# Kernel optimization log

Measured on AMD Instinct MI355X. Metric: run time of the kernel, lower is better.

## Reference

```python
import jax, jax.numpy as jnp
import numpy as np

NUM_Q = 10000
DK = 128   # dim_key (width of each memory slot and of embeddings)
DV = 64    # dim_value (number of memory slots)
B = 128
S = 200


def setup_inputs() -> dict:
    key = jax.random.key(0)
    ks = jax.random.split(key, 16)
    sc = 0.05
    return {
        "question_seq": jax.random.randint(ks[0], (B, S), 0, NUM_Q),
        "correct_seq": jax.random.randint(ks[1], (B, S), 0, 2),
        "k_emb": jax.random.normal(ks[2], (NUM_Q, DK), jnp.float32) * sc,
        "v_emb": jax.random.normal(ks[3], (2 * NUM_Q, DK), jnp.float32) * sc,
        "Mk": jax.random.normal(ks[4], (DV, DK), jnp.float32) * sc,
        "Mv0": jax.random.normal(ks[5], (DV, DK), jnp.float32) * sc,
        "fW": jax.random.normal(ks[6], (2 * DK, DK), jnp.float32) * sc,
        "fb": jnp.zeros((DK,), jnp.float32),
        "eW": jax.random.normal(ks[7], (DK, DK), jnp.float32) * sc,
        "eb": jnp.zeros((DK,), jnp.float32),
        "aW": jax.random.normal(ks[8], (DK, DK), jnp.float32) * sc,
        "ab": jnp.zeros((DK,), jnp.float32),
        "pW": jax.random.normal(ks[9], (DK, 1), jnp.float32) * sc,
        "pb": jnp.zeros((1,), jnp.float32),
    }


def reference(question_seq, correct_seq, k_emb, v_emb, Mk, Mv0, fW, fb, eW, eb, aW, ab, pW, pb):
    num_q = k_emb.shape[0]
    x = question_seq + num_q * correct_seq            # [B,S]
    k = k_emb[question_seq]                           # [B,S,DK]
    v = v_emb[x]                                      # [B,S,DK]

    w = jax.nn.softmax(jnp.einsum('bsk,vk->bsv', k, Mk), axis=-1)  # [B,S,DV]
    e = jax.nn.sigmoid(v @ eW + eb)                   # [B,S,DK]
    a = jnp.tanh(v @ aW + ab)                         # [B,S,DK]

    Mvt0 = jnp.broadcast_to(Mv0[None], (question_seq.shape[0],) + Mv0.shape)  # [B,DV,DK]

    def step(Mvt, inp):
        wt, et, at = inp                              # [B,DV],[B,DK],[B,DK]
        read = jnp.einsum('bv,bvk->bk', wt, Mvt)      # read BEFORE update (Mv[:, :-1])
        we = wt[:, :, None] * et[:, None, :]          # [B,DV,DK]
        wa = wt[:, :, None] * at[:, None, :]
        Mvt_new = Mvt * (1.0 - we) + wa
        return Mvt_new, read

    xs = (w.transpose(1, 0, 2), e.transpose(1, 0, 2), a.transpose(1, 0, 2))
    _, reads = jax.lax.scan(step, Mvt0, xs)           # reads: [S,B,DK]
    reads = reads.transpose(1, 0, 2)                  # [B,S,DK]

    f = jnp.tanh(jnp.concatenate([reads, k], axis=-1) @ fW + fb)  # [B,S,DK]
    # dropout is identity in eval mode
    predict_score = jax.nn.sigmoid(f @ pW + pb).squeeze(-1)       # [B,S]
    return predict_score
```

## Files before the change

kernel.cpp:

```cpp
#include <hip/hip_runtime.h>
#include <math.h>


typedef float f32x4 __attribute__((ext_vector_type(4)));
typedef short bf16x8 __attribute__((ext_vector_type(8)));

__device__ __forceinline__ float sigm(float x) { return 1.0f / (1.0f + __expf(-x)); }
__device__ __forceinline__ float ftanh(float x) {
    x = fminf(20.f, fmaxf(-20.f, x));
    const float t = __expf(2.0f * x);
    return (t - 1.0f) / (t + 1.0f);
}
__device__ __forceinline__ short f2bf(float x) {
    union { float f; unsigned u; } v; v.f = x;
    return (short)((v.u + 0x7FFFu + ((v.u >> 16) & 1u)) >> 16);
}

__global__ __launch_bounds__(256) void prep_kernel(
    const float* __restrict__ eW, const float* __restrict__ aW,
    const float* __restrict__ fW, const float* __restrict__ Mk,
    short* __restrict__ eWt, short* __restrict__ aWt,
    short* __restrict__ fWrt, short* __restrict__ fWkt,
    short* __restrict__ Mkb)
{
    const int t = threadIdx.x;
    if (blockIdx.x == 4) {
        for (int idx = t; idx < 1024; idx += 256) {
            const int row = idx >> 4, c8 = idx & 15;
            const float4 f0 = *(const float4*)(Mk + row * 128 + c8 * 8);
            const float4 f1 = *(const float4*)(Mk + row * 128 + c8 * 8 + 4);
            bf16x8 v;
            v[0] = f2bf(f0.x); v[1] = f2bf(f0.y); v[2] = f2bf(f0.z); v[3] = f2bf(f0.w);
            v[4] = f2bf(f1.x); v[5] = f2bf(f1.y); v[6] = f2bf(f1.z); v[7] = f2bf(f1.w);
            *(bf16x8*)(Mkb + row * 128 + c8 * 8) = v;
        }
        return;
    }
    const float* src; short* dst;
    switch (blockIdx.x) {
        case 0:  src = eW;             dst = eWt;  break;
        case 1:  src = aW;             dst = aWt;  break;
        case 2:  src = fW;             dst = fWrt; break;
        default: src = fW + 128 * 128; dst = fWkt; break;
    }
    const int n  = t & 127;
    const int kh = (t >> 7) * 64;
    for (int k0 = kh; k0 < kh + 64; k0 += 8) {
        bf16x8 v;
        #pragma unroll
        for (int kk = 0; kk < 8; ++kk) v[kk] = f2bf(src[(k0 + kk) * 128 + n]);
        *(bf16x8*)(dst + n * 128 + k0) = v;
    }
}

__global__ __launch_bounds__(256) void veakf_kernel(
    const float* __restrict__ v_emb, const float* __restrict__ k_emb,
    const short* __restrict__ eWt, const short* __restrict__ aWt,
    const short* __restrict__ fWkt, const short* __restrict__ Mkb,
    const float* __restrict__ eb, const float* __restrict__ ab,
    const float* __restrict__ fb,
    int num_q, int nbe, int nbk,
    float* __restrict__ e_all, float* __restrict__ a_all,
    float* __restrict__ kf_all, float* __restrict__ w_all)
{
    __shared__ __align__(16) short Bsh[128 * 128];
    const int t = threadIdx.x;
    const int bid = blockIdx.x;
    int type, R0;
    if (bid < nbe)                { type = 0; R0 = bid * 64; }
    else if (bid < 2 * nbe)       { type = 1; R0 = (bid - nbe) * 64; }
    else if (bid < 2 * nbe + nbk) { type = 2; R0 = (bid - 2 * nbe) * 64; }
    else                          { type = 3; R0 = (bid - 2 * nbe - nbk) * 64; }
    const bool ea = (type < 2);
    const int nrows = ea ? 2 * num_q : num_q;
    const float* Asrc = ea ? v_emb : k_emb;

    const int wv = t >> 6;
    const int lr = t & 15;
    const int lk = (t & 63) >> 4;
    const int arow = wv * 16 + lr;
    int gr = R0 + arow; if (gr > nrows - 1) gr = nrows - 1;

    float4 a0[4], a1[4];
    #pragma unroll
    for (int ks = 0; ks < 4; ++ks) {
        const int off = (ks * 4 + lk) * 8;
        a0[ks] = *(const float4*)(Asrc + (size_t)gr * 128 + off);
        a1[ks] = *(const float4*)(Asrc + (size_t)gr * 128 + off + 4);
    }
    {
        const short* Bt = (type == 0) ? eWt : (type == 1) ? aWt
                        : (type == 2) ? fWkt : Mkb;
        const int niter = (type == 3) ? 4 : 8;
        for (int i = 0; i < niter; ++i) {
            const int c = t + 256 * i;
            const int row = c >> 4, ch = c & 15;
            *(bf16x8*)&Bsh[row * 128 + ((ch ^ (row & 7)) * 8)] =
                *(const bf16x8*)(Bt + row * 128 + ch * 8);
        }
    }
    bf16x8 af[4];
    #pragma unroll
    for (int ks = 0; ks < 4; ++ks) {
        bf16x8 v;
        v[0] = f2bf(a0[ks].x); v[1] = f2bf(a0[ks].y);
        v[2] = f2bf(a0[ks].z); v[3] = f2bf(a0[ks].w);
        v[4] = f2bf(a1[ks].x); v[5] = f2bf(a1[ks].y);
        v[6] = f2bf(a1[ks].z); v[7] = f2bf(a1[ks].w);
        af[ks] = v;
    }
    __syncthreads();

    if (type == 3) {
        f32x4 accw[4];
        #pragma unroll
        for (int ct = 0; ct < 4; ++ct) accw[ct] = (f32x4)0.f;
        #pragma unroll
        for (int ks = 0; ks < 4; ++ks) {
            const int chunk = ks * 4 + lk;
            #pragma unroll
            for (int ct = 0; ct < 4; ++ct) {
                const int n = ct * 16 + lr;
                const bf16x8 b = *(const bf16x8*)&Bsh[n * 128 + ((chunk ^ (n & 7)) * 8)];
                accw[ct] = __builtin_amdgcn_mfma_f32_16x16x32_bf16(af[ks], b, accw[ct], 0, 0, 0);
            }
        }
        #pragma unroll
        for (int r = 0; r < 4; ++r) {
            const float x0 = accw[0][r], x1 = accw[1][r];
            const float x2 = accw[2][r], x3 = accw[3][r];
            float m = fmaxf(fmaxf(x0, x1), fmaxf(x2, x3));
            #pragma unroll
            for (int mk = 1; mk < 16; mk <<= 1) m = fmaxf(m, __shfl_xor(m, mk));
            const float e0 = __expf(x0 - m), e1 = __expf(x1 - m);
            const float e2 = __expf(x2 - m), e3 = __expf(x3 - m);
            float s = (e0 + e1) + (e2 + e3);
            #pragma unroll
            for (int mk = 1; mk < 16; mk <<= 1) s += __shfl_xor(s, mk);
            const float inv = 1.0f / s;
            const int row = R0 + wv * 16 + lk * 4 + r;
            if (row < nrows) {
                float* wr = w_all + (size_t)row * 64 + lr;
                wr[0]  = e0 * inv; wr[16] = e1 * inv;
                wr[32] = e2 * inv; wr[48] = e3 * inv;
            }
        }
        return;
    }

    f32x4 acc[8];
    #pragma unroll
    for (int ct = 0; ct < 8; ++ct) acc[ct] = (f32x4)0.f;
    #pragma unroll
    for (int ks = 0; ks < 4; ++ks) {
        const int chunk = ks * 4 + lk;
        #pragma unroll
        for (int ct = 0; ct < 8; ++ct) {
            const int n = ct * 16 + lr;
            const bf16x8 b = *(const bf16x8*)&Bsh[n * 128 + ((chunk ^ (n & 7)) * 8)];
            acc[ct] = __builtin_amdgcn_mfma_f32_16x16x32_bf16(af[ks], b, acc[ct], 0, 0, 0);
        }
    }
    #pragma unroll
    for (int ct = 0; ct < 8; ++ct) {
        const int col = ct * 16 + lr;
        #pragma unroll
        for (int r = 0; r < 4; ++r) {
            const int row = R0 + wv * 16 + lk * 4 + r;
            if (row < nrows) {
                if (type == 0)
                    e_all[(size_t)row * 128 + col]  = sigm(acc[ct][r] + eb[col]);
                else if (type == 1)
                    a_all[(size_t)row * 128 + col]  = ftanh(acc[ct][r] + ab[col]);
                else
                    kf_all[(size_t)row * 128 + col] = acc[ct][r] + fb[col];
            }
        }
    }
}

__global__ __launch_bounds__(256) void scan_kernel(
    const float* __restrict__ Mv0,
    const int* __restrict__ qseq, const int* __restrict__ cseq,
    const float* __restrict__ w_all, const float* __restrict__ e_all,
    const float* __restrict__ a_all, int num_q,
    unsigned short* __restrict__ reads_bf)
{
    const int t  = threadIdx.x;
    const int j  = t & 31;
    const int vg = t >> 5;
    const int cq = blockIdx.x & 3;
    const int b  = blockIdx.x >> 2;
    const int jg = cq * 32 + j;

    float Mv[8];
    #pragma unroll
    for (int i = 0; i < 8; ++i) Mv[i] = Mv0[(vg * 8 + i) * 128 + jg];

    __shared__ float wb[2][8][64];
    __shared__ float ebuf[2][8][32];
    __shared__ float abuf[2][8][32];
    __shared__ float part[2][8][8][32];
    __shared__ int sq[200], sx[200];

    if (t < 200) {
        const int q = qseq[b * 200 + t];
        const int c = cseq[b * 200 + t];
        sq[t] = q * 16;
        sx[t] = (q + num_q * c) * 32 + cq * 8;
    }
    __syncthreads();

    const float4* w4 = (const float4*)w_all;
    const float4* e4 = (const float4*)e_all;
    const float4* a4 = (const float4*)a_all;

    float4 rg;
    if (t < 128)      { rg = w4[sq[t >> 4] + (t & 15)];                       ((float4*)wb[0])[t] = rg; }
    else if (t < 192) { const int u = t - 128; rg = e4[sx[u >> 3] + (u & 7)]; ((float4*)ebuf[0])[u] = rg; }
    else              { const int u = t - 192; rg = a4[sx[u >> 3] + (u & 7)]; ((float4*)abuf[0])[u] = rg; }
    __syncthreads();

    int cb = 0, pbuf = 0;
    for (int c = 0; c < 25; ++c) {
        if (c < 24) {
            const int s0 = (c + 1) * 8;
            if (t < 128)      rg = w4[sq[s0 + (t >> 4)] + (t & 15)];
            else if (t < 192) { const int u = t - 128; rg = e4[sx[s0 + (u >> 3)] + (u & 7)]; }
            else              { const int u = t - 192; rg = a4[sx[s0 + (u >> 3)] + (u & 7)]; }
        }
        #pragma unroll
        for (int st = 0; st < 8; ++st) {
            const float e_j = ebuf[cb][st][j];
            const float a_j = abuf[cb][st][j];
            const float* wrow = &wb[cb][st][vg * 8];
            float r0 = 0.f, r1 = 0.f, r2 = 0.f, r3 = 0.f;
            #pragma unroll
            for (int v4i = 0; v4i < 2; ++v4i) {
                const float4 w4v = *(const float4*)&wrow[v4i * 4];
                const int v = v4i * 4;
                r0 = fmaf(w4v.x, Mv[v + 0], r0);
                Mv[v + 0] = fmaf(w4v.x, fmaf(-Mv[v + 0], e_j, a_j), Mv[v + 0]);
                r1 = fmaf(w4v.y, Mv[v + 1], r1);
                Mv[v + 1] = fmaf(w4v.y, fmaf(-Mv[v + 1], e_j, a_j), Mv[v + 1]);
                r2 = fmaf(w4v.z, Mv[v + 2], r2);
                Mv[v + 2] = fmaf(w4v.z, fmaf(-Mv[v + 2], e_j, a_j), Mv[v + 2]);
                r3 = fmaf(w4v.w, Mv[v + 3], r3);
                Mv[v + 3] = fmaf(w4v.w, fmaf(-Mv[v + 3], e_j, a_j), Mv[v + 3]);
            }
            part[pbuf][st][vg][j] = (r0 + r1) + (r2 + r3);
        }
        if (c < 24) {
            if (t < 128)      ((float4*)wb[cb ^ 1])[t] = rg;
            else if (t < 192) ((float4*)ebuf[cb ^ 1])[t - 128] = rg;
            else              ((float4*)abuf[cb ^ 1])[t - 192] = rg;
        }
        __syncthreads();
        {
            const int st = t >> 5, jr = t & 31;
            const float* pp = &part[pbuf][st][0][jr];
            float r = 0.f;
            #pragma unroll
            for (int g = 0; g < 8; ++g) r += pp[g * 32];
            reads_bf[(size_t)b * 200 * 128 + (size_t)(c * 8 + st) * 128 + cq * 32 + jr]
                = (unsigned short)f2bf(r);
        }
        cb ^= 1; pbuf ^= 1;
    }
}

__global__ __launch_bounds__(256) void out_kernel(
    const int* __restrict__ qseq,
    const unsigned short* __restrict__ reads_bf,
    const short* __restrict__ fWrt, const float* __restrict__ kf_all,
    const float* __restrict__ pW, const float* __restrict__ pb,
    int ntok, float* __restrict__ out)
{
    __shared__ __align__(16) short Ash[64 * 128];
    __shared__ int qi[64];
    const int t = threadIdx.x;
    const int R0 = blockIdx.x * 64;
    if (t < 64) { int r = R0 + t; qi[t] = qseq[r < ntok ? r : ntok - 1]; }
    #pragma unroll
    for (int i = 0; i < 4; ++i) {
        const int c = t + 256 * i;
        const int row = c >> 4, ch = c & 15;
        int gr = R0 + row; if (gr > ntok - 1) gr = ntok - 1;
        const bf16x8 v = *(const bf16x8*)(reads_bf + (size_t)gr * 128 + ch * 8);
        *(bf16x8*)&Ash[row * 128 + ((ch ^ (row & 7)) * 8)] = v;
    }
    __syncthreads();

    const int wv = t >> 6;
    const int lr = t & 15;
    const int lk = (t & 63) >> 4;
    const int arow = wv * 16 + lr;

    f32x4 acc[8];
    #pragma unroll
    for (int ct = 0; ct < 8; ++ct) {
        const int col = ct * 16 + lr;
        #pragma unroll
        for (int r = 0; r < 4; ++r) {
            const int q = qi[wv * 16 + lk * 4 + r];
            acc[ct][r] = kf_all[(size_t)q * 128 + col];
        }
    }
    #pragma unroll
    for (int ks = 0; ks < 4; ++ks) {
        const int chunk = ks * 4 + lk;
        const bf16x8 af = *(const bf16x8*)&Ash[arow * 128 + ((chunk ^ (arow & 7)) * 8)];
        const int kb = ks * 32 + lk * 8;
        #pragma unroll
        for (int ct = 0; ct < 8; ++ct) {
            const int n = ct * 16 + lr;
            const bf16x8 bfr = *(const bf16x8*)(fWrt + n * 128 + kb);
            acc[ct] = __builtin_amdgcn_mfma_f32_16x16x32_bf16(af, bfr, acc[ct], 0, 0, 0);
        }
    }
    const float pb0 = pb[0];
    float s0 = 0.f, s1 = 0.f, s2 = 0.f, s3 = 0.f;
    #pragma unroll
    for (int ct = 0; ct < 8; ++ct) {
        const float pw = pW[ct * 16 + lr];
        s0 = fmaf(ftanh(acc[ct][0]), pw, s0);
        s1 = fmaf(ftanh(acc[ct][1]), pw, s1);
        s2 = fmaf(ftanh(acc[ct][2]), pw, s2);
        s3 = fmaf(ftanh(acc[ct][3]), pw, s3);
    }
    #pragma unroll
    for (int off = 1; off < 16; off <<= 1) {
        s0 += __shfl_xor(s0, off);
        s1 += __shfl_xor(s1, off);
        s2 += __shfl_xor(s2, off);
        s3 += __shfl_xor(s3, off);
    }
    if (lr == 0) {
        const int row = R0 + wv * 16 + lk * 4;
        if (row + 0 < ntok) out[row + 0] = sigm(s0 + pb0);
        if (row + 1 < ntok) out[row + 1] = sigm(s1 + pb0);
        if (row + 2 < ntok) out[row + 2] = sigm(s2 + pb0);
        if (row + 3 < ntok) out[row + 3] = sigm(s3 + pb0);
    }
}

extern "C" void kernel_launch(void* const* d_in, const int* in_sizes, int n_in,
                              void* d_out, int out_size, void* d_ws, size_t ws_size,
                              hipStream_t stream)
{
    const int*   qseq  = (const int*)d_in[0];
    const int*   cseq  = (const int*)d_in[1];
    const float* k_emb = (const float*)d_in[2];
    const float* v_emb = (const float*)d_in[3];
    const float* Mk    = (const float*)d_in[4];
    const float* Mv0   = (const float*)d_in[5];
    const float* fW    = (const float*)d_in[6];
    const float* fb    = (const float*)d_in[7];
    const float* eW    = (const float*)d_in[8];
    const float* eb    = (const float*)d_in[9];
    const float* aW    = (const float*)d_in[10];
    const float* ab    = (const float*)d_in[11];
    const float* pW    = (const float*)d_in[12];
    const float* pb    = (const float*)d_in[13];

    const int num_q = in_sizes[2] / 128;
    const int ntok  = in_sizes[0];
    const int Bb    = ntok / 200;
    const int NV    = 2 * num_q;

    float* ws = (float*)d_ws;
    float* w_all  = ws;
    float* e_all  = w_all  + (size_t)num_q * 64;
    float* a_all  = e_all  + (size_t)NV * 128;
    float* kf_all = a_all  + (size_t)NV * 128;
    short* eWt    = (short*)(kf_all + (size_t)num_q * 128);
    short* aWt    = eWt  + 128 * 128;
    short* fWrt   = aWt  + 128 * 128;
    short* fWkt   = fWrt + 128 * 128;
    short* Mkb    = fWkt + 128 * 128;
    unsigned short* reads_bf = (unsigned short*)(Mkb + 64 * 128);

    prep_kernel<<<5, 256, 0, stream>>>(eW, aW, fW, Mk, eWt, aWt, fWrt, fWkt, Mkb);
    const int nbe = (NV + 63) / 64, nbk = (num_q + 63) / 64;
    veakf_kernel<<<2 * nbe + 2 * nbk, 256, 0, stream>>>(
        v_emb, k_emb, eWt, aWt, fWkt, Mkb, eb, ab, fb, num_q, nbe, nbk,
        e_all, a_all, kf_all, w_all);
    scan_kernel<<<Bb * 4, 256, 0, stream>>>(Mv0, qseq, cseq, w_all, e_all, a_all,
                                            num_q, reads_bf);
    out_kernel<<<(ntok + 63) / 64, 256, 0, stream>>>(qseq, reads_bf, fWrt, kf_all,
                                                     pW, pb, ntok, (float*)d_out);
}
```

Before: 72.63 us.

## Store e/a tables in bf16 via LDS-staged coalesced epilogue, double-buffer B fragments

The e and a projection tables are now written as bf16 instead of fp32. The epilogue stages the accumulators through shared memory so each thread writes coalesced 16-byte rows, and bias is loaded into LDS. The scan kernel gathers the half-size bf16 rows and converts them to float in shared memory, which halves the gather traffic. The MFMA loop also double-buffers B fragments in registers and adds a min-blocks launch bound. The cost is lower precision on e and a, plus leftover dead code in the epilogue.

```diff
diff --git a/kernel.cpp b/kernel.cpp
--- a/kernel.cpp
+++ b/kernel.cpp
@@ -14,6 +14,10 @@
 __device__ __forceinline__ short f2bf(float x) {
     union { float f; unsigned u; } v; v.f = x;
     return (short)((v.u + 0x7FFFu + ((v.u >> 16) & 1u)) >> 16);
+}
+__device__ __forceinline__ float bf2f(short h) {
+    union { unsigned u; float f; } v; v.u = ((unsigned)(unsigned short)h) << 16;
+    return v.f;
 }
 
 __global__ __launch_bounds__(256) void prep_kernel(
@@ -53,17 +57,21 @@
     }
 }
 
-__global__ __launch_bounds__(256) void veakf_kernel(
+__global__ __launch_bounds__(256, 2) void veakf_kernel(
     const float* __restrict__ v_emb, const float* __restrict__ k_emb,
     const short* __restrict__ eWt, const short* __restrict__ aWt,
     const short* __restrict__ fWkt, const short* __restrict__ Mkb,
     const float* __restrict__ eb, const float* __restrict__ ab,
     const float* __restrict__ fb,
     int num_q, int nbe, int nbk,
-    float* __restrict__ e_all, float* __restrict__ a_all,
+    unsigned short* __restrict__ e_bf, unsigned short* __restrict__ a_bf,
     float* __restrict__ kf_all, float* __restrict__ w_all)
 {
-    __shared__ __align__(16) short Bsh[128 * 128];
+    __shared__ __align__(16) char smem[64 * 132 * 4];
+    short* Bsh = (short*)smem;
+    float* Fsh = (float*)smem;
+    __shared__ float biasL[128];
+
     const int t = threadIdx.x;
     const int bid = blockIdx.x;
     int type, R0;
@@ -99,6 +107,10 @@
                 *(const bf16x8*)(Bt + row * 128 + ch * 8);
         }
     }
+    if (ea && t < 32) {
+        const float* bsrc = (type == 0) ? eb : ab;
+        *(float4*)&biasL[t * 4] = *(const float4*)(bsrc + t * 4);
+    }
     bf16x8 af[4];
     #pragma unroll
     for (int ks = 0; ks < 4; ++ks) {
@@ -151,39 +163,125 @@
     f32x4 acc[8];
     #pragma unroll
     for (int ct = 0; ct < 8; ++ct) acc[ct] = (f32x4)0.f;
+
+    bf16x8 bA[8], bB[8];
+    #pragma unroll
+    for (int ct = 0; ct < 8; ++ct) {
+        const int n = ct * 16 + lr;
+        bA[ct] = *(const bf16x8*)&Bsh[n * 128 + (((0 * 4 + lk) ^ (n & 7)) * 8)];
+    }
     #pragma unroll
     for (int ks = 0; ks < 4; ++ks) {
-        const int chunk = ks * 4 + lk;
+        if (ks < 3) {
+            const int chunk = (ks + 1) * 4 + lk;
+            if ((ks & 1) == 0) {
+                #pragma unroll
+                for (int ct = 0; ct < 8; ++ct) {
+                    const int n = ct * 16 + lr;
+                    bB[ct] = *(const bf16x8*)&Bsh[n * 128 + ((chunk ^ (n & 7)) * 8)];
+                }
+            } else {
+                #pragma unroll
+                for (int ct = 0; ct < 8; ++ct) {
+                    const int n = ct * 16 + lr;
+                    bA[ct] = *(const bf16x8*)&Bsh[n * 128 + ((chunk ^ (n & 7)) * 8)];
+                }
+            }
+        }
+        if ((ks & 1) == 0) {
+            #pragma unroll
+            for (int ct = 0; ct < 8; ++ct)
+                acc[ct] = __builtin_amdgcn_mfma_f32_16x16x32_bf16(af[ks], bA[ct], acc[ct], 0, 0, 0);
+        } else {
+            #pragma unroll
+            for (int ct = 0; ct < 8; ++ct)
+                acc[ct] = __builtin_amdgcn_mfma_f32_16x16x32_bf16(af[ks], bB[ct], acc[ct], 0, 0, 0);
+        }
+    }
+
+    if (type == 2) {
         #pragma unroll
         for (int ct = 0; ct < 8; ++ct) {
-            const int n = ct * 16 + lr;
-            const bf16x8 b = *(const bf16x8*)&Bsh[n * 128 + ((chunk ^ (n & 7)) * 8)];
-            acc[ct] = __builtin_amdgcn_mfma_f32_16x16x32_bf16(af[ks], b, acc[ct], 0, 0, 0);
-        }
-    }
+            const int col = ct * 16 + lr;
+            #pragma unroll
+            for (int r = 0; r < 4; ++r) {
+                const int row = R0 + wv * 16 + lk * 4 + r;
+                if (row < nrows)
+                    kf_all[(size_t)row * 128 + col] = acc[ct][r] + fb[col];
+            }
+        }
+        return;
+    }
+
+    __syncthreads();
     #pragma unroll
     for (int ct = 0; ct < 8; ++ct) {
         const int col = ct * 16 + lr;
-        #pragma unroll
-        for (int r = 0; r < 4; ++r) {
-            const int row = R0 + wv * 16 + lk * 4 + r;
-            if (row < nrows) {
-                if (type == 0)
-                    e_all[(size_t)row * 128 + col]  = sigm(acc[ct][r] + eb[col]);
-                else if (type == 1)
-                    a_all[(size_t)row * 128 + col]  = ftanh(acc[ct][r] + ab[col]);
-                else
-                    kf_all[(size_t)row * 128 + col] = acc[ct][r] + fb[col];
-            }
-        }
+        const int rbase = wv * 16 + lk * 4;
+        Fsh[(rbase + 0) * 132 + col] = acc[ct][0];
+        Fsh[(rbase + 1) * 132 + col] = acc[ct][1];
+        Fsh[(rbase + 2) * 132 + col] = acc[ct][2];
+        Fsh[(rbase + 3) * 132 + col] = acc[ct][3];
+    }
+    __syncthreads();
+    unsigned short* dst = (type == 0) ? e_bf : a_bf;
+    #pragma unroll
+    for (int i = 0; i < 2; ++i) {
+        const int idx = t + 256 * i;
+        const int row = idx >> 3, ch = idx & 7;
+        const int grow = R0 + row;
+        float v[8];
+        #pragma unroll
+        for (int kk = 0; kk < 8; ++kk)
+            v[kk] = Fsh[row * 132 + ch * 16 + kk * 2 + (i ^ (kk & 0))] ;
+        (void)v;
+        bf16x8 o;
+        if (type == 0) {
+            #pragma unroll
+            for (int kk = 0; kk < 8; ++kk) {
+                const int c = ch * 16 + kk;
+                (void)c;
+            }
+        }
+        if (i == 0 || i == 1) {
+            const int row2 = idx >> 4, ch2 = idx & 15;
+            const int grow2 = R0 + row2;
+            bf16x8 o2;
+            #pragma unroll
+            for (int kk = 0; kk < 8; ++kk) {
+                const int c = ch2 * 8 + kk;
+                float x = Fsh[row2 * 132 + c] + biasL[c];
+                x = (type == 0) ? sigm(x) : ftanh(x);
+                o2[kk] = f2bf(x);
+            }
+            if (grow2 < nrows)
+                *(bf16x8*)(dst + (size_t)grow2 * 128 + ch2 * 8) = o2;
+        }
+        (void)grow; (void)o;
+    }
+    #pragma unroll
+    for (int i = 2; i < 4; ++i) {
+        const int idx = t + 256 * i;
+        const int row2 = idx >> 4, ch2 = idx & 15;
+        const int grow2 = R0 + row2;
+        bf16x8 o2;
+        #pragma unroll
+        for (int kk = 0; kk < 8; ++kk) {
+            const int c = ch2 * 8 + kk;
+            float x = Fsh[row2 * 132 + c] + biasL[c];
+            x = (type == 0) ? sigm(x) : ftanh(x);
+            o2[kk] = f2bf(x);
+        }
+        if (grow2 < nrows)
+            *(bf16x8*)(dst + (size_t)grow2 * 128 + ch2 * 8) = o2;
     }
 }
 
 __global__ __launch_bounds__(256) void scan_kernel(
     const float* __restrict__ Mv0,
     const int* __restrict__ qseq, const int* __restrict__ cseq,
-    const float* __restrict__ w_all, const float* __restrict__ e_all,
-    const float* __restrict__ a_all, int num_q,
+    const float* __restrict__ w_all, const unsigned short* __restrict__ e_bf,
+    const unsigned short* __restrict__ a_bf, int num_q,
     unsigned short* __restrict__ reads_bf)
 {
     const int t  = threadIdx.x;
@@ -207,27 +305,38 @@
         const int q = qseq[b * 200 + t];
         const int c = cseq[b * 200 + t];
         sq[t] = q * 16;
-        sx[t] = (q + num_q * c) * 32 + cq * 8;
+        sx[t] = (q + num_q * c) * 16 + cq * 4;
     }
     __syncthreads();
 
     const float4* w4 = (const float4*)w_all;
-    const float4* e4 = (const float4*)e_all;
-    const float4* a4 = (const float4*)a_all;
-
-    float4 rg;
-    if (t < 128)      { rg = w4[sq[t >> 4] + (t & 15)];                       ((float4*)wb[0])[t] = rg; }
-    else if (t < 192) { const int u = t - 128; rg = e4[sx[u >> 3] + (u & 7)]; ((float4*)ebuf[0])[u] = rg; }
-    else              { const int u = t - 192; rg = a4[sx[u >> 3] + (u & 7)]; ((float4*)abuf[0])[u] = rg; }
+    const bf16x8* e8 = (const bf16x8*)e_bf;
+    const bf16x8* a8 = (const bf16x8*)a_bf;
+
+    float4 rgw; bf16x8 rgh;
+    if (t < 128) {
+        rgw = w4[sq[t >> 4] + (t & 15)];
+        ((float4*)wb[0])[t] = rgw;
+    } else if (t < 160) {
+        const int u = t - 128; rgh = e8[sx[u >> 2] + (u & 3)];
+        float* d = &ebuf[0][u >> 2][(u & 3) * 8];
+        #pragma unroll
+        for (int k = 0; k < 8; ++k) d[k] = bf2f(rgh[k]);
+    } else if (t < 192) {
+        const int u = t - 160; rgh = a8[sx[u >> 2] + (u & 3)];
+        float* d = &abuf[0][u >> 2][(u & 3) * 8];
+        #pragma unroll
+        for (int k = 0; k < 8; ++k) d[k] = bf2f(rgh[k]);
+    }
     __syncthreads();
 
     int cb = 0, pbuf = 0;
     for (int c = 0; c < 25; ++c) {
         if (c < 24) {
             const int s0 = (c + 1) * 8;
-            if (t < 128)      rg = w4[sq[s0 + (t >> 4)] + (t & 15)];
-            else if (t < 192) { const int u = t - 128; rg = e4[sx[s0 + (u >> 3)] + (u & 7)]; }
-            else              { const int u = t - 192; rg = a4[sx[s0 + (u >> 3)] + (u & 7)]; }
+            if (t < 128)      rgw = w4[sq[s0 + (t >> 4)] + (t & 15)];
+            else if (t < 160) { const int u = t - 128; rgh = e8[sx[s0 + (u >> 2)] + (u & 3)]; }
+            else if (t < 192) { const int u = t - 160; rgh = a8[sx[s0 + (u >> 2)] + (u & 3)]; }
         }
         #pragma unroll
         for (int st = 0; st < 8; ++st) {
@@ -251,9 +360,18 @@
             part[pbuf][st][vg][j] = (r0 + r1) + (r2 + r3);
         }
         if (c < 24) {
-            if (t < 128)      ((float4*)wb[cb ^ 1])[t] = rg;
-            else if (t < 192) ((float4*)ebuf[cb ^ 1])[t - 128] = rg;
-            else              ((float4*)abuf[cb ^ 1])[t - 192] = rg;
+            if (t < 128)      ((float4*)wb[cb ^ 1])[t] = rgw;
+            else if (t < 160) {
+                const int u = t - 128;
+                float* d = &ebuf[cb ^ 1][u >> 2][(u & 3) * 8];
+                #pragma unroll
+                for (int k = 0; k < 8; ++k) d[k] = bf2f(rgh[k]);
+            } else if (t < 192) {
+                const int u = t - 160;
+                float* d = &abuf[cb ^ 1][u >> 2][(u & 3) * 8];
+                #pragma unroll
+                for (int k = 0; k < 8; ++k) d[k] = bf2f(rgh[k]);
+            }
         }
         __syncthreads();
         {
@@ -370,22 +488,22 @@
 
     float* ws = (float*)d_ws;
     float* w_all  = ws;
-    float* e_all  = w_all  + (size_t)num_q * 64;
-    float* a_all  = e_all  + (size_t)NV * 128;
-    float* kf_all = a_all  + (size_t)NV * 128;
+    float* kf_all = w_all + (size_t)num_q * 64;
     short* eWt    = (short*)(kf_all + (size_t)num_q * 128);
     short* aWt    = eWt  + 128 * 128;
     short* fWrt   = aWt  + 128 * 128;
     short* fWkt   = fWrt + 128 * 128;
     short* Mkb    = fWkt + 128 * 128;
-    unsigned short* reads_bf = (unsigned short*)(Mkb + 64 * 128);
+    unsigned short* e_bf = (unsigned short*)(Mkb + 64 * 128);
+    unsigned short* a_bf = e_bf + (size_t)NV * 128;
+    unsigned short* reads_bf = a_bf + (size_t)NV * 128;
 
     prep_kernel<<<5, 256, 0, stream>>>(eW, aW, fW, Mk, eWt, aWt, fWrt, fWkt, Mkb);
     const int nbe = (NV + 63) / 64, nbk = (num_q + 63) / 64;
     veakf_kernel<<<2 * nbe + 2 * nbk, 256, 0, stream>>>(
         v_emb, k_emb, eWt, aWt, fWkt, Mkb, eb, ab, fb, num_q, nbe, nbk,
-        e_all, a_all, kf_all, w_all);
-    scan_kernel<<<Bb * 4, 256, 0, stream>>>(Mv0, qseq, cseq, w_all, e_all, a_all,
+        e_bf, a_bf, kf_all, w_all);
+    scan_kernel<<<Bb * 4, 256, 0, stream>>>(Mv0, qseq, cseq, w_all, e_bf, a_bf,
                                             num_q, reads_bf);
     out_kernel<<<(ntok + 63) / 64, 256, 0, stream>>>(qseq, reads_bf, fWrt, kf_all,
                                                      pW, pb, ntok, (float*)d_out);
```

Result: slower. 76.47 us (+5.3%).
